# Kernel tuning notes

Hardware: AMD Instinct MI355X
Metric: run time of the kernel (lower is better)

Reference implementation:

```python
import jax, jax.numpy as jnp
import numpy as np

B, L, T = 8, 4096, 128
D_H, D_G, D_PROJ = 1024, 256, 256


def setup_inputs() -> dict:
    key = jax.random.key(0)
    k1, k2, k3, k4, k5 = jax.random.split(key, 5)
    H = jax.random.normal(k1, (B, L, D_H), dtype=jnp.float32)
    G = jax.random.normal(k2, (B, T, D_G), dtype=jnp.float32)
    mask = jax.random.randint(k3, (B, L), 0, 2) == 1  # True = masked out
    Wk = jax.random.normal(k4, (D_H, D_PROJ), dtype=jnp.float32) * 0.02
    Wq = jax.random.normal(k5, (D_G, D_PROJ), dtype=jnp.float32) * 0.02
    return {"H": H, "G": G, "mask": mask, "Wk": Wk, "Wq": Wq}


def reference(H, G, mask, Wk, Wq):
    scale = D_PROJ ** (-0.5)
    K = jnp.einsum('bld,dp->blp', H, Wk)          # [B, L, d_proj]
    Q = jnp.einsum('btd,dp->btp', G, Wq)          # [B, T, d_proj]
    logits = jnp.einsum('btp,blp->btl', Q, K) * scale  # [B, T, L]
    logits = jnp.where(mask[:, None, :], -jnp.inf, logits)
    alpha = jax.nn.softmax(logits, axis=-1)       # [B, T, L]
    Z = jnp.einsum('btl,bld->btd', alpha, H)      # [B, T, d_h]
    return Z
```

## Files before the change

### kernel.cpp

```cpp
#include <hip/hip_runtime.h>
#include <hip/hip_bf16.h>
#include <math.h>

#define B_  8
#define L_  4096
#define T_  128
#define DH  1024
#define DG  256
#define DP  256
#define BK  64

typedef short bf16x8 __attribute__((ext_vector_type(8)));
typedef float f32x4  __attribute__((ext_vector_type(4)));

#define AS1(p) ((const __attribute__((address_space(1))) void*)(p))
#define AS3(p) ((__attribute__((address_space(3))) void*)(p))

__device__ __forceinline__ unsigned short f2bf(float f) {
    unsigned u = __float_as_uint(f);
    unsigned r = (u + 0x7FFFu + ((u >> 16) & 1u)) >> 16;
    return (unsigned short)r;
}

__global__ __launch_bounds__(256) void qk_kernel(const float* __restrict__ G,
                                                 const float* __restrict__ Wq,
                                                 const float* __restrict__ Wk,
                                                 unsigned short* __restrict__ Qk) {
    __shared__ float Gs[DG];
    __shared__ float Qs[DP];
    const int bt  = blockIdx.x;
    const int tid = threadIdx.x;

    Gs[tid] = G[(size_t)bt * DG + tid];
    __syncthreads();
    float q = 0.f;
    #pragma unroll 4
    for (int g = 0; g < DG; ++g) q += Gs[g] * Wq[(size_t)g * DP + tid];
    Qs[tid] = q * 0.0625f;
    __syncthreads();

    const int t = tid & 15, dsub = tid >> 4;
    for (int pass = 0; pass < 64; ++pass) {
        const int d = pass * 16 + dsub;
        const float* w = Wk + (size_t)d * DP + t * 16;
        float s = 0.f;
        #pragma unroll
        for (int i = 0; i < 16; ++i) s += Qs[t * 16 + i] * w[i];
        s += __shfl_down(s, 8, 64);
        s += __shfl_down(s, 4, 64);
        s += __shfl_down(s, 2, 64);
        s += __shfl_down(s, 1, 64);
        if (t == 0) Qk[(size_t)bt * DH + d] = f2bf(s);
    }
}

__global__ __launch_bounds__(256) void logits_kernel(const unsigned short* __restrict__ Qk,
                                                     const float* __restrict__ H,
                                                     float* __restrict__ logits) {
    __shared__ __attribute__((aligned(16))) unsigned short As[T_ * BK];
    __shared__ __attribute__((aligned(16))) unsigned short Bs[64 * BK];
    const int b = blockIdx.y, l0 = blockIdx.x * 64;
    const int tid = threadIdx.x, wave = tid >> 6, lane = tid & 63;
    const unsigned short* Ab = Qk + (size_t)b * T_ * DH;
    const float*          Hb = H + ((size_t)b * L_ + l0) * DH;

    const int lm = lane & 15, quad = lane >> 4;
    const int wm = wave >> 1, wn = wave & 1;
    f32x4 acc[4][2] = {};

    const int ar = lane >> 3, akb = (lane & 7) * 8;
    const int bc = (tid & 15) * 4, br0 = tid >> 4;

    for (int k0 = 0; k0 < DH; k0 += BK) {
        #pragma unroll
        for (int s = 0; s < 4; ++s) {
            const int rowb = s * 32 + wave * 8;
            const unsigned short* gp = Ab + (size_t)(rowb + ar) * DH + k0 + akb;
            __builtin_amdgcn_global_load_lds(AS1(gp), AS3(&As[rowb * BK]), 16, 0, 0);
        }
        #pragma unroll
        for (int s = 0; s < 4; ++s) {
            const int row = br0 + s * 16;
            const float4 v = *(const float4*)(Hb + (size_t)row * DH + k0 + bc);
            ushort4 p;
            p.x = f2bf(v.x); p.y = f2bf(v.y); p.z = f2bf(v.z); p.w = f2bf(v.w);
            *(ushort4*)(&Bs[row * BK + bc]) = p;
        }
        __syncthreads();
        #pragma unroll
        for (int ks = 0; ks < 2; ++ks) {
            bf16x8 a[4], bf[2];
            #pragma unroll
            for (int i = 0; i < 4; ++i)
                a[i] = *(const bf16x8*)(&As[(wm * 64 + i * 16 + lm) * BK + ks * 32 + quad * 8]);
            #pragma unroll
            for (int j = 0; j < 2; ++j)
                bf[j] = *(const bf16x8*)(&Bs[(wn * 32 + j * 16 + lm) * BK + ks * 32 + quad * 8]);
            #pragma unroll
            for (int i = 0; i < 4; ++i)
                #pragma unroll
                for (int j = 0; j < 2; ++j)
                    acc[i][j] = __builtin_amdgcn_mfma_f32_16x16x32_bf16(a[i], bf[j], acc[i][j], 0, 0, 0);
        }
        __syncthreads();
    }
    float* Cb = logits + (size_t)b * T_ * L_ + l0;
    #pragma unroll
    for (int i = 0; i < 4; ++i)
        #pragma unroll
        for (int j = 0; j < 2; ++j)
            #pragma unroll
            for (int r = 0; r < 4; ++r)
                Cb[(size_t)(wm * 64 + i * 16 + quad * 4 + r) * L_ + wn * 32 + j * 16 + lm] = acc[i][j][r];
}

__global__ __launch_bounds__(256) void softmax_kernel(const float* __restrict__ logits,
                                                      const int* __restrict__ mask,
                                                      unsigned short* __restrict__ alpha) {
    const int row = blockIdx.x;
    const int b   = row >> 7;
    const int tid = threadIdx.x;
    const float* ptr = logits + (size_t)row * L_;
    const int* mrow = mask + (size_t)b * L_;

    float vals[16];
    float vmax = -3.0e38f;
    #pragma unroll
    for (int s = 0; s < 16; ++s) {
        const int l = tid + s * 256;
        float v = ptr[l];
        v = mrow[l] ? -3.0e38f : v;
        vals[s] = v;
        vmax = fmaxf(vmax, v);
    }
    #pragma unroll
    for (int off = 32; off; off >>= 1) vmax = fmaxf(vmax, __shfl_down(vmax, off, 64));

    __shared__ float red[4];
    __shared__ float bcast;
    const int wid = tid >> 6, lane = tid & 63;
    if (lane == 0) red[wid] = vmax;
    __syncthreads();
    if (tid == 0) bcast = fmaxf(fmaxf(red[0], red[1]), fmaxf(red[2], red[3]));
    __syncthreads();
    const float m = bcast;

    float sum = 0.f;
    #pragma unroll
    for (int s = 0; s < 16; ++s) {
        vals[s] = __expf(vals[s] - m);
        sum += vals[s];
    }
    #pragma unroll
    for (int off = 32; off; off >>= 1) sum += __shfl_down(sum, off, 64);
    __syncthreads();
    if (lane == 0) red[wid] = sum;
    __syncthreads();
    if (tid == 0) bcast = red[0] + red[1] + red[2] + red[3];
    __syncthreads();
    const float inv = 1.0f / bcast;

    unsigned short* arow = alpha + (size_t)row * L_;
    #pragma unroll
    for (int s = 0; s < 16; ++s) arow[tid + s * 256] = f2bf(vals[s] * inv);
}

__global__ __launch_bounds__(256) void z_kernel(const unsigned short* __restrict__ alpha,
                                                const float* __restrict__ H,
                                                float* __restrict__ partials) {
    __shared__ __attribute__((aligned(16))) unsigned short As[T_ * BK];
    __shared__ __attribute__((aligned(16))) unsigned short Bs[64 * (BK + 2)];
    const int d0 = blockIdx.x * 64, b = blockIdx.y, ch = blockIdx.z;
    const int tid = threadIdx.x, wave = tid >> 6, lane = tid & 63;
    const int Lc = L_ / 4;
    const unsigned short* Ab = alpha + (size_t)b * T_ * L_ + ch * Lc;
    const float*          Hb = H + ((size_t)b * L_ + ch * Lc) * DH + d0;

    const int lm = lane & 15, quad = lane >> 4;
    const int wm = wave >> 1, wn = wave & 1;
    f32x4 acc[4][2] = {};

    const int ar = lane >> 3, akb = (lane & 7) * 8;
    const int dg = tid & 7, lp = tid >> 3;

    unsigned* B32 = (unsigned*)Bs;

    for (int k0 = 0; k0 < Lc; k0 += BK) {
        #pragma unroll
        for (int s = 0; s < 4; ++s) {
            const int rowb = s * 32 + wave * 8;
            const unsigned short* gp = Ab + (size_t)(rowb + ar) * L_ + k0 + akb;
            __builtin_amdgcn_global_load_lds(AS1(gp), AS3(&As[rowb * BK]), 16, 0, 0);
        }
        {
            const float* r0 = Hb + (size_t)(k0 + 2 * lp) * DH + dg * 8;
            const float4 v0a = *(const float4*)(r0);
            const float4 v0b = *(const float4*)(r0 + 4);
            const float4 v1a = *(const float4*)(r0 + DH);
            const float4 v1b = *(const float4*)(r0 + DH + 4);
            float a0[8] = {v0a.x, v0a.y, v0a.z, v0a.w, v0b.x, v0b.y, v0b.z, v0b.w};
            float a1[8] = {v1a.x, v1a.y, v1a.z, v1a.w, v1b.x, v1b.y, v1b.z, v1b.w};
            #pragma unroll
            for (int i = 0; i < 8; ++i) {
                const int d = dg * 8 + i;
                B32[d * 33 + lp] = (unsigned)f2bf(a0[i]) | ((unsigned)f2bf(a1[i]) << 16);
            }
        }
        __syncthreads();
        #pragma unroll
        for (int ks = 0; ks < 2; ++ks) {
            bf16x8 a[4], bf[2];
            #pragma unroll
            for (int i = 0; i < 4; ++i)
                a[i] = *(const bf16x8*)(&As[(wm * 64 + i * 16 + lm) * BK + ks * 32 + quad * 8]);
            #pragma unroll
            for (int j = 0; j < 2; ++j) {
                const int d = wn * 32 + j * 16 + lm;
                const unsigned* p = B32 + d * 33 + ks * 16 + quad * 4;
                union { bf16x8 v; unsigned u[4]; } f;
                f.u[0] = p[0]; f.u[1] = p[1]; f.u[2] = p[2]; f.u[3] = p[3];
                bf[j] = f.v;
            }
            #pragma unroll
            for (int i = 0; i < 4; ++i)
                #pragma unroll
                for (int j = 0; j < 2; ++j)
                    acc[i][j] = __builtin_amdgcn_mfma_f32_16x16x32_bf16(a[i], bf[j], acc[i][j], 0, 0, 0);
        }
        __syncthreads();
    }
    float* Cb = partials + (((size_t)ch * B_ + b) * T_) * DH + d0;
    #pragma unroll
    for (int i = 0; i < 4; ++i)
        #pragma unroll
        for (int j = 0; j < 2; ++j)
            #pragma unroll
            for (int r = 0; r < 4; ++r)
                Cb[(size_t)(wm * 64 + i * 16 + quad * 4 + r) * DH + wn * 32 + j * 16 + lm] = acc[i][j][r];
}

__global__ __launch_bounds__(256) void reduce_kernel(const float* __restrict__ p,
                                                     float* __restrict__ Z) {
    const size_t n = (size_t)B_ * T_ * DH;
    const size_t i = ((size_t)blockIdx.x * 256 + threadIdx.x) * 4;
    const float4 a = *(const float4*)(p + i);
    const float4 b = *(const float4*)(p + n + i);
    const float4 c = *(const float4*)(p + 2 * n + i);
    const float4 d = *(const float4*)(p + 3 * n + i);
    float4 o;
    o.x = a.x + b.x + c.x + d.x;
    o.y = a.y + b.y + c.y + d.y;
    o.z = a.z + b.z + c.z + d.z;
    o.w = a.w + b.w + c.w + d.w;
    *(float4*)(Z + i) = o;
}

extern "C" void kernel_launch(void* const* d_in, const int* in_sizes, int n_in,
                              void* d_out, int out_size, void* d_ws, size_t ws_size,
                              hipStream_t stream) {
    const float* H    = (const float*)d_in[0];
    const float* G    = (const float*)d_in[1];
    const int*   mask = (const int*)d_in[2];
    const float* Wk   = (const float*)d_in[3];
    const float* Wq   = (const float*)d_in[4];
    float* Z = (float*)d_out;

    char* ws = (char*)d_ws;
    unsigned short* Qk     = (unsigned short*)ws;
    float*          logits = (float*)(ws + ((size_t)2  << 20));
    unsigned short* alpha  = (unsigned short*)(ws + ((size_t)18 << 20));
    float*          parts  = (float*)(ws + ((size_t)26 << 20));

    qk_kernel<<<B_ * T_, 256, 0, stream>>>(G, Wq, Wk, Qk);
    logits_kernel<<<dim3(L_ / 64, B_), 256, 0, stream>>>(Qk, H, logits);
    softmax_kernel<<<B_ * T_, 256, 0, stream>>>(logits, mask, alpha);
    z_kernel<<<dim3(DH / 64, B_, 4), 256, 0, stream>>>(alpha, H, parts);
    reduce_kernel<<<(B_ * T_ * DH / 4) / 256, 256, 0, stream>>>(parts, Z);
}
```

Measured before the change: 337.5 us.

## Reassociate Q·Wkᵀ into combined weight GEMM, vectorize softmax, atomic-reduce Z

Replaces the scalar per-row Q/Wk projection kernel with two MFMA GEMMs: first Wk·Wqᵀ into a bf16 combined weight (scaled), then G times that weight to produce Qk. The softmax kernel now uses float4/int4 loads and ushort4 stores. The separate partial-sum reduction kernel is removed: z_kernel atomically adds its four L-chunk partials into a zeroed output. The aim is to cut the slow scalar projection and one extra launch plus its partials traffic, at the cost of an extra bf16 rounding of the combined weight and nondeterministic float atomics.

```diff
diff --git a/kernel.cpp b/kernel.cpp
--- a/kernel.cpp
+++ b/kernel.cpp
@@ -22,36 +22,116 @@
     return (unsigned short)r;
 }
 
-__global__ __launch_bounds__(256) void qk_kernel(const float* __restrict__ G,
-                                                 const float* __restrict__ Wq,
-                                                 const float* __restrict__ Wk,
-                                                 unsigned short* __restrict__ Qk) {
-    __shared__ float Gs[DG];
-    __shared__ float Qs[DP];
-    const int bt  = blockIdx.x;
-    const int tid = threadIdx.x;
-
-    Gs[tid] = G[(size_t)bt * DG + tid];
-    __syncthreads();
-    float q = 0.f;
-    #pragma unroll 4
-    for (int g = 0; g < DG; ++g) q += Gs[g] * Wq[(size_t)g * DP + tid];
-    Qs[tid] = q * 0.0625f;
-    __syncthreads();
-
-    const int t = tid & 15, dsub = tid >> 4;
-    for (int pass = 0; pass < 64; ++pass) {
-        const int d = pass * 16 + dsub;
-        const float* w = Wk + (size_t)d * DP + t * 16;
-        float s = 0.f;
-        #pragma unroll
-        for (int i = 0; i < 16; ++i) s += Qs[t * 16 + i] * w[i];
-        s += __shfl_down(s, 8, 64);
-        s += __shfl_down(s, 4, 64);
-        s += __shfl_down(s, 2, 64);
-        s += __shfl_down(s, 1, 64);
-        if (t == 0) Qk[(size_t)bt * DH + d] = f2bf(s);
-    }
+__global__ __launch_bounds__(256) void wct_kernel(const float* __restrict__ Wk,
+                                                  const float* __restrict__ Wq,
+                                                  unsigned short* __restrict__ Wct) {
+    __shared__ __attribute__((aligned(16))) unsigned short As[128 * BK];
+    __shared__ __attribute__((aligned(16))) unsigned short Bs[64 * BK];
+    const int n0 = blockIdx.x * 64, m0 = blockIdx.y * 128;
+    const int tid = threadIdx.x, wave = tid >> 6, lane = tid & 63;
+    const int lm = lane & 15, quad = lane >> 4;
+    const int wm = wave >> 1, wn = wave & 1;
+    const int bc = (tid & 15) * 4, br = tid >> 4;
+    f32x4 acc[4][2] = {};
+
+    for (int k0 = 0; k0 < DP; k0 += BK) {
+        #pragma unroll
+        for (int s = 0; s < 8; ++s) {
+            const int row = br + s * 16;
+            const float4 v = *(const float4*)(Wk + (size_t)(m0 + row) * DP + k0 + bc);
+            ushort4 p; p.x = f2bf(v.x); p.y = f2bf(v.y); p.z = f2bf(v.z); p.w = f2bf(v.w);
+            *(ushort4*)(&As[row * BK + bc]) = p;
+        }
+        #pragma unroll
+        for (int s = 0; s < 4; ++s) {
+            const int row = br + s * 16;
+            const float4 v = *(const float4*)(Wq + (size_t)(n0 + row) * DP + k0 + bc);
+            ushort4 p; p.x = f2bf(v.x); p.y = f2bf(v.y); p.z = f2bf(v.z); p.w = f2bf(v.w);
+            *(ushort4*)(&Bs[row * BK + bc]) = p;
+        }
+        __syncthreads();
+        #pragma unroll
+        for (int ks = 0; ks < 2; ++ks) {
+            bf16x8 a[4], bf[2];
+            #pragma unroll
+            for (int i = 0; i < 4; ++i)
+                a[i] = *(const bf16x8*)(&As[(wm * 64 + i * 16 + lm) * BK + ks * 32 + quad * 8]);
+            #pragma unroll
+            for (int j = 0; j < 2; ++j)
+                bf[j] = *(const bf16x8*)(&Bs[(wn * 32 + j * 16 + lm) * BK + ks * 32 + quad * 8]);
+            #pragma unroll
+            for (int i = 0; i < 4; ++i)
+                #pragma unroll
+                for (int j = 0; j < 2; ++j)
+                    acc[i][j] = __builtin_amdgcn_mfma_f32_16x16x32_bf16(a[i], bf[j], acc[i][j], 0, 0, 0);
+        }
+        __syncthreads();
+    }
+    unsigned short* Cb = Wct + (size_t)m0 * DG + n0;
+    #pragma unroll
+    for (int i = 0; i < 4; ++i)
+        #pragma unroll
+        for (int j = 0; j < 2; ++j)
+            #pragma unroll
+            for (int r = 0; r < 4; ++r)
+                Cb[(size_t)(wm * 64 + i * 16 + quad * 4 + r) * DG + wn * 32 + j * 16 + lm] =
+                    f2bf(acc[i][j][r] * 0.0625f);
+}
+
+__global__ __launch_bounds__(256) void qproj_kernel(const float* __restrict__ G,
+                                                    const unsigned short* __restrict__ Wct,
+                                                    unsigned short* __restrict__ Qk) {
+    __shared__ __attribute__((aligned(16))) unsigned short As[128 * BK];
+    __shared__ __attribute__((aligned(16))) unsigned short Bs[64 * BK];
+    const int n0 = blockIdx.x * 64, m0 = blockIdx.y * 128;
+    const int tid = threadIdx.x, wave = tid >> 6, lane = tid & 63;
+    const int lm = lane & 15, quad = lane >> 4;
+    const int wm = wave >> 1, wn = wave & 1;
+    const int bc = (tid & 15) * 4, br = tid >> 4;
+    const int ar = lane >> 3, akb = (lane & 7) * 8;
+    f32x4 acc[4][2] = {};
+
+    for (int k0 = 0; k0 < DG; k0 += BK) {
+        #pragma unroll
+        for (int s = 0; s < 8; ++s) {
+            const int row = br + s * 16;
+            const float4 v = *(const float4*)(G + (size_t)(m0 + row) * DG + k0 + bc);
+            ushort4 p; p.x = f2bf(v.x); p.y = f2bf(v.y); p.z = f2bf(v.z); p.w = f2bf(v.w);
+            *(ushort4*)(&As[row * BK + bc]) = p;
+        }
+        #pragma unroll
+        for (int s = 0; s < 2; ++s) {
+            const int rowb = s * 32 + wave * 8;
+            const unsigned short* gp = Wct + (size_t)(n0 + rowb + ar) * DG + k0 + akb;
+            __builtin_amdgcn_global_load_lds(AS1(gp), AS3(&Bs[rowb * BK]), 16, 0, 0);
+        }
+        __syncthreads();
+        #pragma unroll
+        for (int ks = 0; ks < 2; ++ks) {
+            bf16x8 a[4], bf[2];
+            #pragma unroll
+            for (int i = 0; i < 4; ++i)
+                a[i] = *(const bf16x8*)(&As[(wm * 64 + i * 16 + lm) * BK + ks * 32 + quad * 8]);
+            #pragma unroll
+            for (int j = 0; j < 2; ++j)
+                bf[j] = *(const bf16x8*)(&Bs[(wn * 32 + j * 16 + lm) * BK + ks * 32 + quad * 8]);
+            #pragma unroll
+            for (int i = 0; i < 4; ++i)
+                #pragma unroll
+                for (int j = 0; j < 2; ++j)
+                    acc[i][j] = __builtin_amdgcn_mfma_f32_16x16x32_bf16(a[i], bf[j], acc[i][j], 0, 0, 0);
+        }
+        __syncthreads();
+    }
+    unsigned short* Cb = Qk + (size_t)m0 * DH + n0;
+    #pragma unroll
+    for (int i = 0; i < 4; ++i)
+        #pragma unroll
+        for (int j = 0; j < 2; ++j)
+            #pragma unroll
+            for (int r = 0; r < 4; ++r)
+                Cb[(size_t)(wm * 64 + i * 16 + quad * 4 + r) * DH + wn * 32 + j * 16 + lm] =
+                    f2bf(acc[i][j][r]);
 }
 
 __global__ __launch_bounds__(256) void logits_kernel(const unsigned short* __restrict__ Qk,
@@ -67,7 +147,6 @@
     const int lm = lane & 15, quad = lane >> 4;
     const int wm = wave >> 1, wn = wave & 1;
     f32x4 acc[4][2] = {};
-
     const int ar = lane >> 3, akb = (lane & 7) * 8;
     const int bc = (tid & 15) * 4, br0 = tid >> 4;
 
@@ -82,8 +161,7 @@
         for (int s = 0; s < 4; ++s) {
             const int row = br0 + s * 16;
             const float4 v = *(const float4*)(Hb + (size_t)row * DH + k0 + bc);
-            ushort4 p;
-            p.x = f2bf(v.x); p.y = f2bf(v.y); p.z = f2bf(v.z); p.w = f2bf(v.w);
+            ushort4 p; p.x = f2bf(v.x); p.y = f2bf(v.y); p.z = f2bf(v.z); p.w = f2bf(v.w);
             *(ushort4*)(&Bs[row * BK + bc]) = p;
         }
         __syncthreads();
@@ -120,18 +198,22 @@
     const int row = blockIdx.x;
     const int b   = row >> 7;
     const int tid = threadIdx.x;
-    const float* ptr = logits + (size_t)row * L_;
-    const int* mrow = mask + (size_t)b * L_;
-
-    float vals[16];
+    const float4* p4 = (const float4*)(logits + (size_t)row * L_);
+    const int4*   m4 = (const int4*)(mask + (size_t)b * L_);
+
+    float vals[4][4];
     float vmax = -3.0e38f;
     #pragma unroll
-    for (int s = 0; s < 16; ++s) {
-        const int l = tid + s * 256;
-        float v = ptr[l];
-        v = mrow[l] ? -3.0e38f : v;
-        vals[s] = v;
-        vmax = fmaxf(vmax, v);
+    for (int s = 0; s < 4; ++s) {
+        const int idx = tid + s * 256;
+        float4 v = p4[idx];
+        const int4 mm = m4[idx];
+        v.x = mm.x ? -3.0e38f : v.x;
+        v.y = mm.y ? -3.0e38f : v.y;
+        v.z = mm.z ? -3.0e38f : v.z;
+        v.w = mm.w ? -3.0e38f : v.w;
+        vals[s][0] = v.x; vals[s][1] = v.y; vals[s][2] = v.z; vals[s][3] = v.w;
+        vmax = fmaxf(vmax, fmaxf(fmaxf(v.x, v.y), fmaxf(v.z, v.w)));
     }
     #pragma unroll
     for (int off = 32; off; off >>= 1) vmax = fmaxf(vmax, __shfl_down(vmax, off, 64));
@@ -147,10 +229,12 @@
 
     float sum = 0.f;
     #pragma unroll
-    for (int s = 0; s < 16; ++s) {
-        vals[s] = __expf(vals[s] - m);
-        sum += vals[s];
-    }
+    for (int s = 0; s < 4; ++s)
+        #pragma unroll
+        for (int i = 0; i < 4; ++i) {
+            vals[s][i] = __expf(vals[s][i] - m);
+            sum += vals[s][i];
+        }
     #pragma unroll
     for (int off = 32; off; off >>= 1) sum += __shfl_down(sum, off, 64);
     __syncthreads();
@@ -162,12 +246,17 @@
 
     unsigned short* arow = alpha + (size_t)row * L_;
     #pragma unroll
-    for (int s = 0; s < 16; ++s) arow[tid + s * 256] = f2bf(vals[s] * inv);
+    for (int s = 0; s < 4; ++s) {
+        ushort4 p;
+        p.x = f2bf(vals[s][0] * inv); p.y = f2bf(vals[s][1] * inv);
+        p.z = f2bf(vals[s][2] * inv); p.w = f2bf(vals[s][3] * inv);
+        *(ushort4*)(arow + (size_t)(tid + s * 256) * 4) = p;
+    }
 }
 
 __global__ __launch_bounds__(256) void z_kernel(const unsigned short* __restrict__ alpha,
                                                 const float* __restrict__ H,
-                                                float* __restrict__ partials) {
+                                                float* __restrict__ Z) {
     __shared__ __attribute__((aligned(16))) unsigned short As[T_ * BK];
     __shared__ __attribute__((aligned(16))) unsigned short Bs[64 * (BK + 2)];
     const int d0 = blockIdx.x * 64, b = blockIdx.y, ch = blockIdx.z;
@@ -179,10 +268,8 @@
     const int lm = lane & 15, quad = lane >> 4;
     const int wm = wave >> 1, wn = wave & 1;
     f32x4 acc[4][2] = {};
-
     const int ar = lane >> 3, akb = (lane & 7) * 8;
     const int dg = tid & 7, lp = tid >> 3;
-
     unsigned* B32 = (unsigned*)Bs;
 
     for (int k0 = 0; k0 < Lc; k0 += BK) {
@@ -229,30 +316,15 @@
         }
         __syncthreads();
     }
-    float* Cb = partials + (((size_t)ch * B_ + b) * T_) * DH + d0;
+    float* Cb = Z + (size_t)b * T_ * DH + d0;
     #pragma unroll
     for (int i = 0; i < 4; ++i)
         #pragma unroll
         for (int j = 0; j < 2; ++j)
             #pragma unroll
             for (int r = 0; r < 4; ++r)
-                Cb[(size_t)(wm * 64 + i * 16 + quad * 4 + r) * DH + wn * 32 + j * 16 + lm] = acc[i][j][r];
-}
-
-__global__ __launch_bounds__(256) void reduce_kernel(const float* __restrict__ p,
-                                                     float* __restrict__ Z) {
-    const size_t n = (size_t)B_ * T_ * DH;
-    const size_t i = ((size_t)blockIdx.x * 256 + threadIdx.x) * 4;
-    const float4 a = *(const float4*)(p + i);
-    const float4 b = *(const float4*)(p + n + i);
-    const float4 c = *(const float4*)(p + 2 * n + i);
-    const float4 d = *(const float4*)(p + 3 * n + i);
-    float4 o;
-    o.x = a.x + b.x + c.x + d.x;
-    o.y = a.y + b.y + c.y + d.y;
-    o.z = a.z + b.z + c.z + d.z;
-    o.w = a.w + b.w + c.w + d.w;
-    *(float4*)(Z + i) = o;
+                atomicAdd(&Cb[(size_t)(wm * 64 + i * 16 + quad * 4 + r) * DH + wn * 32 + j * 16 + lm],
+                          acc[i][j][r]);
 }
 
 extern "C" void kernel_launch(void* const* d_in, const int* in_sizes, int n_in,
@@ -266,14 +338,15 @@
     float* Z = (float*)d_out;
 
     char* ws = (char*)d_ws;
-    unsigned short* Qk     = (unsigned short*)ws;
-    float*          logits = (float*)(ws + ((size_t)2  << 20));
-    unsigned short* alpha  = (unsigned short*)(ws + ((size_t)18 << 20));
-    float*          parts  = (float*)(ws + ((size_t)26 << 20));
-
-    qk_kernel<<<B_ * T_, 256, 0, stream>>>(G, Wq, Wk, Qk);
+    unsigned short* Wct    = (unsigned short*)ws;
+    unsigned short* Qk     = (unsigned short*)(ws + ((size_t)1 << 20));
+    float*          logits = (float*)(ws + ((size_t)4 << 20));
+    unsigned short* alpha  = (unsigned short*)(ws + ((size_t)24 << 20));
+
+    hipMemsetAsync(Z, 0, (size_t)out_size * sizeof(float), stream);
+    wct_kernel<<<dim3(DG / 64, DH / 128), 256, 0, stream>>>(Wk, Wq, Wct);
+    qproj_kernel<<<dim3(DH / 64, (B_ * T_) / 128), 256, 0, stream>>>(G, Wct, Qk);
     logits_kernel<<<dim3(L_ / 64, B_), 256, 0, stream>>>(Qk, H, logits);
     softmax_kernel<<<B_ * T_, 256, 0, stream>>>(logits, mask, alpha);
-    z_kernel<<<dim3(DH / 64, B_, 4), 256, 0, stream>>>(alpha, H, parts);
-    reduce_kernel<<<(B_ * T_ * DH / 4) / 256, 256, 0, stream>>>(parts, Z);
-}
+    z_kernel<<<dim3(DH / 64, B_, 4), 256, 0, stream>>>(alpha, H, Z);
+}
```

Result: faster. 285.4 us (-15.5%).
